# Performance work log

Hardware: AMD Instinct MI355X
Metric: run time of the kernel (lower is better)

Reference implementation:

```python
import jax, jax.numpy as jnp
import numpy as np

B, N, DEG = 256, 16384, 32  # batch, num_neurons, fan-in per neuron

def setup_inputs() -> dict:
    key = jax.random.key(0)
    kx, kw, ki = jax.random.split(key, 3)
    x = jax.random.normal(kx, (B, N), dtype=jnp.float32)
    w = jax.random.normal(kw, (N, DEG), dtype=jnp.float32)  # nonzero weights per neuron
    idx = jax.random.randint(ki, (N, DEG), 0, N)            # source-neuron indices per neuron
    return {"x": x, "w": w, "idx": idx}

def reference(x, w, idx):
    # Per neuron j: gather its fan-in channels and apply Dense(1) with
    # kernel = nonzero weights, then relu; concat over neurons == axis N.
    gathered = x[:, idx]                      # [B, N, DEG] gather
    out = jnp.einsum('bnd,nd->bn', gathered, w)  # sparse matvec per batch row
    return jax.nn.relu(out)                   # [B, N]
```

## Files before the change

kernel.cpp:

```cpp
#include <hip/hip_runtime.h>


#define NB   16384
#define DEG  32

typedef __fp16 hp2 __attribute__((ext_vector_type(2)));

__device__ __forceinline__ unsigned pk16(float a, float b) {
    return __builtin_bit_cast(unsigned, (hp2)__builtin_amdgcn_cvt_pkrtz(a, b));
}

__global__ __launch_bounds__(256) void prep_kernel(
    const int* __restrict__ idx, const float* __restrict__ w,
    const float* __restrict__ x, uint2* __restrict__ pw,
    uint2* __restrict__ xq) {
    __shared__ int   idx_s[64][33];
    __shared__ float w_s[64][33];
    const int t = threadIdx.x;

    if (blockIdx.x < 4096) {
        const int jt = (int)blockIdx.x & 63;
        const int q  = (int)blockIdx.x >> 6;
        const int j  = jt * 256 + t;
        const float* xr = x + (size_t)(4 * q) * NB + j;
        const float a0 = xr[0];
        const float a1 = xr[NB];
        const float a2 = xr[2 * NB];
        const float a3 = xr[3 * NB];
        uint2 o;
        o.x = pk16(a0, a1);
        o.y = pk16(a2, a3);
        xq[((size_t)q << 14) + j] = o;
        return;
    }

    const int nb = ((int)blockIdx.x - 4096) * 64;
    const int4*   src  = (const int4*)(idx + (size_t)nb * DEG);
    const float4* srcw = (const float4*)(w   + (size_t)nb * DEG);
#pragma unroll
    for (int p = 0; p < 2; ++p) {
        const int e4 = t + 256 * p;
        const int n0 = e4 >> 3;
        const int c0 = (e4 & 7) * 4;
        const int4 v = src[e4];
        idx_s[n0][c0 + 0] = v.x; idx_s[n0][c0 + 1] = v.y;
        idx_s[n0][c0 + 2] = v.z; idx_s[n0][c0 + 3] = v.w;
        const float4 f = srcw[e4];
        w_s[n0][c0 + 0] = f.x; w_s[n0][c0 + 1] = f.y;
        w_s[n0][c0 + 2] = f.z; w_s[n0][c0 + 3] = f.w;
    }
    __syncthreads();

    const int np    = t & 63;
    const int dbase = t >> 6;
#pragma unroll
    for (int k = 0; k < 4; ++k) {
        const int d2 = dbase * 4 + k;
        uint2 o;
        o.x = (unsigned)idx_s[np][2 * d2] | ((unsigned)idx_s[np][2 * d2 + 1] << 16);
        o.y = pk16(w_s[np][2 * d2], w_s[np][2 * d2 + 1]);
        pw[(size_t)d2 * NB + nb + np] = o;
    }
}

__global__ __launch_bounds__(1024) void gather4_kernel(
    const uint2* __restrict__ xq, const uint2* __restrict__ pw,
    float* __restrict__ out) {
    extern __shared__ uint2 lds[];
    const int t  = threadIdx.x;
    const int q  = (int)blockIdx.x >> 2;
    const int n0 = ((int)blockIdx.x & 3) * 4096;

    {
        const uint4* src = (const uint4*)(xq + ((size_t)q << 14));
        uint4* dst = (uint4*)lds;
#pragma unroll
        for (int i = 0; i < 8; ++i) dst[t + 1024 * i] = src[t + 1024 * i];
    }
    __syncthreads();

    const int b0 = 4 * q;
    for (int i = 0; i < 4; ++i) {
        const int n = n0 + t + 1024 * i;
        uint2 qd[16];
#pragma unroll
        for (int d2 = 0; d2 < 16; ++d2)
            qd[d2] = pw[(size_t)d2 * NB + n];

        hp2 a01 = {0, 0}, a23 = {0, 0}, c01 = {0, 0}, c23 = {0, 0};
#pragma unroll
        for (int d2 = 0; d2 < 8; ++d2) {
            const unsigned jp = qd[d2].x;
            const uint2 g0 = lds[jp & 0xffffu];
            const uint2 g1 = lds[jp >> 16];
            const hp2 w2 = __builtin_bit_cast(hp2, qd[d2].y);
            const hp2 wlo = {w2.x, w2.x};
            const hp2 whi = {w2.y, w2.y};
            a01 += wlo * __builtin_bit_cast(hp2, g0.x);
            a23 += wlo * __builtin_bit_cast(hp2, g0.y);
            a01 += whi * __builtin_bit_cast(hp2, g1.x);
            a23 += whi * __builtin_bit_cast(hp2, g1.y);
        }
#pragma unroll
        for (int d2 = 8; d2 < 16; ++d2) {
            const unsigned jp = qd[d2].x;
            const uint2 g0 = lds[jp & 0xffffu];
            const uint2 g1 = lds[jp >> 16];
            const hp2 w2 = __builtin_bit_cast(hp2, qd[d2].y);
            const hp2 wlo = {w2.x, w2.x};
            const hp2 whi = {w2.y, w2.y};
            c01 += wlo * __builtin_bit_cast(hp2, g0.x);
            c23 += wlo * __builtin_bit_cast(hp2, g0.y);
            c01 += whi * __builtin_bit_cast(hp2, g1.x);
            c23 += whi * __builtin_bit_cast(hp2, g1.y);
        }
        const hp2 s01 = a01 + c01;
        const hp2 s23 = a23 + c23;
        out[(size_t)(b0 + 0) * NB + n] = fmaxf((float)s01.x, 0.f);
        out[(size_t)(b0 + 1) * NB + n] = fmaxf((float)s01.y, 0.f);
        out[(size_t)(b0 + 2) * NB + n] = fmaxf((float)s23.x, 0.f);
        out[(size_t)(b0 + 3) * NB + n] = fmaxf((float)s23.y, 0.f);
    }
}

extern "C" void kernel_launch(void* const* d_in, const int* in_sizes, int n_in,
                              void* d_out, int out_size, void* d_ws, size_t ws_size,
                              hipStream_t stream) {
    const float* x   = (const float*)d_in[0];
    const float* w   = (const float*)d_in[1];
    const int*   idx = (const int*)d_in[2];
    float* out = (float*)d_out;
    uint2* pw  = (uint2*)d_ws;
    uint2* xq  = (uint2*)((char*)d_ws + (2u << 20));

    (void)hipFuncSetAttribute((const void*)gather4_kernel,
                              hipFuncAttributeMaxDynamicSharedMemorySize, 131072);

    prep_kernel<<<4096 + NB / 64, 256, 0, stream>>>(idx, w, x, pw, xq);

    gather4_kernel<<<256, 1024, 131072, stream>>>(xq, pw, out);
}
```

Baseline: 90.61 us.

## Fuse x fp16 packing into gather kernel and drop intermediate xq buffer

The separate prep pass that converted four batch rows of x to packed fp16 and wrote them to a workspace buffer is removed. The gather kernel now reads the four fp32 rows directly with float4 loads and packs them into LDS itself, so the xq round trip through global memory and 4096 prep blocks go away. The block-to-work mapping is also reordered so consecutive blocks share the same neuron range across different batch quads, and launch bounds gain a minimum-occupancy hint. In exchange, each of the 4 blocks working on the same batch quad now converts x redundantly, reading 4x more fp32 data than the old packed copy.

```diff
diff --git a/kernel.cpp b/kernel.cpp
--- a/kernel.cpp
+++ b/kernel.cpp
@@ -10,31 +10,14 @@
     return __builtin_bit_cast(unsigned, (hp2)__builtin_amdgcn_cvt_pkrtz(a, b));
 }
 
-__global__ __launch_bounds__(256) void prep_kernel(
+__global__ __launch_bounds__(256) void prep_pw_kernel(
     const int* __restrict__ idx, const float* __restrict__ w,
-    const float* __restrict__ x, uint2* __restrict__ pw,
-    uint2* __restrict__ xq) {
+    uint2* __restrict__ pw) {
     __shared__ int   idx_s[64][33];
     __shared__ float w_s[64][33];
-    const int t = threadIdx.x;
+    const int t  = threadIdx.x;
+    const int nb = (int)blockIdx.x * 64;
 
-    if (blockIdx.x < 4096) {
-        const int jt = (int)blockIdx.x & 63;
-        const int q  = (int)blockIdx.x >> 6;
-        const int j  = jt * 256 + t;
-        const float* xr = x + (size_t)(4 * q) * NB + j;
-        const float a0 = xr[0];
-        const float a1 = xr[NB];
-        const float a2 = xr[2 * NB];
-        const float a3 = xr[3 * NB];
-        uint2 o;
-        o.x = pk16(a0, a1);
-        o.y = pk16(a2, a3);
-        xq[((size_t)q << 14) + j] = o;
-        return;
-    }
-
-    const int nb = ((int)blockIdx.x - 4096) * 64;
     const int4*   src  = (const int4*)(idx + (size_t)nb * DEG);
     const float4* srcw = (const float4*)(w   + (size_t)nb * DEG);
 #pragma unroll
@@ -63,19 +46,32 @@
     }
 }
 
-__global__ __launch_bounds__(1024) void gather4_kernel(
-    const uint2* __restrict__ xq, const uint2* __restrict__ pw,
+__global__ __launch_bounds__(1024, 4) void gather4_kernel(
+    const float* __restrict__ x, const uint2* __restrict__ pw,
     float* __restrict__ out) {
     extern __shared__ uint2 lds[];
     const int t  = threadIdx.x;
-    const int q  = (int)blockIdx.x >> 2;
-    const int n0 = ((int)blockIdx.x & 3) * 4096;
+    const int q  = (int)blockIdx.x & 63;
+    const int n0 = ((int)blockIdx.x >> 6) * 4096;
 
-    {
-        const uint4* src = (const uint4*)(xq + ((size_t)q << 14));
-        uint4* dst = (uint4*)lds;
+    const float* xr0 = x + (size_t)(4 * q) * NB;
+    const float* xr1 = xr0 + NB;
+    const float* xr2 = xr1 + NB;
+    const float* xr3 = xr2 + NB;
 #pragma unroll
-        for (int i = 0; i < 8; ++i) dst[t + 1024 * i] = src[t + 1024 * i];
+    for (int p = 0; p < 4; ++p) {
+        const int j = 4 * (t + 1024 * p);
+        const float4 r0 = *(const float4*)&xr0[j];
+        const float4 r1 = *(const float4*)&xr1[j];
+        const float4 r2 = *(const float4*)&xr2[j];
+        const float4 r3 = *(const float4*)&xr3[j];
+        uint4 w0, w1;
+        w0.x = pk16(r0.x, r1.x); w0.y = pk16(r2.x, r3.x);
+        w0.z = pk16(r0.y, r1.y); w0.w = pk16(r2.y, r3.y);
+        w1.x = pk16(r0.z, r1.z); w1.y = pk16(r2.z, r3.z);
+        w1.z = pk16(r0.w, r1.w); w1.w = pk16(r2.w, r3.w);
+        *(uint4*)&lds[j]     = w0;
+        *(uint4*)&lds[j + 2] = w1;
     }
     __syncthreads();
 
@@ -131,12 +127,11 @@
     const int*   idx = (const int*)d_in[2];
     float* out = (float*)d_out;
     uint2* pw  = (uint2*)d_ws;
-    uint2* xq  = (uint2*)((char*)d_ws + (2u << 20));
 
     (void)hipFuncSetAttribute((const void*)gather4_kernel,
                               hipFuncAttributeMaxDynamicSharedMemorySize, 131072);
 
-    prep_kernel<<<4096 + NB / 64, 256, 0, stream>>>(idx, w, x, pw, xq);
+    prep_pw_kernel<<<NB / 64, 256, 0, stream>>>(idx, w, pw);
 
-    gather4_kernel<<<256, 1024, 131072, stream>>>(xq, pw, out);
+    gather4_kernel<<<256, 1024, 131072, stream>>>(x, pw, out);
 }
```

New measurement: 84.75 us. -6.5%, faster.
